# Kernel tuning notes

Measured on AMD Instinct MI355X. Metric: run time of the kernel, lower is better.

## Reference

```python
import jax, jax.numpy as jnp
import numpy as np

T, B, N, F = 128, 8, 32, 128
H = 256  # hidden channels
DEG = 8


def setup_inputs() -> dict:
    key = jax.random.key(0)
    ks = jax.random.split(key, 8)
    data = jax.random.normal(ks[0], (T, B, N, F), jnp.float32)
    all_ohs = jax.random.normal(ks[1], (T, B, N, 8), jnp.float32)
    n0 = B * N * T
    n1 = B * N * (T // 2)
    edge_index0 = jax.random.randint(ks[2], (2, n0 * DEG), 0, n0)
    edge_index1 = jax.random.randint(ks[3], (2, n1 * DEG), 0, n1)
    def init(k, shape, fan):
        return jax.random.normal(k, shape, jnp.float32) / np.float32(np.sqrt(fan))
    W0 = init(ks[4], (2 * F, H), 2 * F); b0 = jnp.zeros((H,), jnp.float32)
    Wc0 = init(ks[5], (H, H, 5), H * 5); bc0 = jnp.zeros((H,), jnp.float32)
    W1 = init(ks[6], (2 * H, H), 2 * H); b1 = jnp.zeros((H,), jnp.float32)
    Wc1 = init(ks[7], (H, H, 5), H * 5); bc1 = jnp.zeros((H,), jnp.float32)
    return dict(data=data, all_ohs=all_ohs,
                edge_index0=edge_index0, edge_index1=edge_index1,
                W0=W0, b0=b0, Wc0=Wc0, bc0=bc0,
                W1=W1, b1=b1, Wc1=Wc1, bc1=bc1)


def edge_conv(x, edge_index, W, b):
    # PyG EdgeConv: out_i = max_{(j->i)} relu(Linear(cat[x_i, x_j - x_i]))
    src, dst = edge_index[0], edge_index[1]
    x_i = x[dst]           # [E, C] target features
    x_j = x[src]           # [E, C] source features
    msg = jax.nn.relu(jnp.concatenate([x_i, x_j - x_i], axis=-1) @ W + b)
    out = jax.ops.segment_max(msg, dst, num_segments=x.shape[0])
    return jnp.where(jnp.isneginf(out), 0.0, out)  # empty segments -> 0 (PyG fill)


def temp_conv(x, Wc, bc):
    # x: [BN, C, L]; Conv1d(k=5, pad=2) + relu + MaxPool1d(2)
    y = jax.lax.conv_general_dilated(x, Wc, (1,), [(2, 2)],
                                     dimension_numbers=('NCH', 'OIH', 'NCH'))
    y = jax.nn.relu(y + bc[None, :, None])
    L2 = y.shape[-1] // 2
    y = y[..., : L2 * 2].reshape(y.shape[0], y.shape[1], L2, 2)
    return jnp.max(y, axis=-1)


def reference(data, all_ohs, edge_index0, edge_index1,
              W0, b0, Wc0, bc0, W1, b1, Wc1, bc1):
    # 'fast' path, context=False: all_ohs unused beyond reshape
    length = data.shape[0]
    x = data.reshape(T, B * N, F).transpose(1, 0, 2).reshape(-1, F)  # [BN*T, F]
    layers = ((edge_index0, W0, b0, Wc0, bc0),
              (edge_index1, W1, b1, Wc1, bc1))
    for ei, W, b, Wc, bc in layers:
        x = edge_conv(x, ei, W, b)                       # [BN*length, C]
        x = x.reshape(-1, length, x.shape[-1])           # [BN, length, C]
        x = x.transpose(0, 2, 1)                         # [BN, C, length]
        x = temp_conv(x, Wc, bc)                         # [BN, C, length//2]
        length = x.shape[2]
        C = x.shape[1]
        x = x.transpose(0, 2, 1).reshape(-1, C)          # [BN*length, C]
    return x
```

## Files before the change

kernel.cpp:

```cpp
#include <hip/hip_runtime.h>
#include <hip/hip_bf16.h>
#include <math.h>

#define T0 128
#define BN 256
#define Ff 128
#define Hh 256
#define NODE0 32768
#define E0 262144
#define T1 64
#define NODE1 16384
#define E1 131072
#define CAP 48

typedef __attribute__((ext_vector_type(8))) short bhalf8;
typedef __attribute__((ext_vector_type(4))) float floatx4;

__device__ __forceinline__ unsigned short f2bf(float x) {
  union { float f; unsigned u; } v; v.f = x;
  unsigned r = v.u + 0x7fff + ((v.u >> 16) & 1);
  return (unsigned short)(r >> 16);
}
__device__ __forceinline__ float bf2f(unsigned short b) {
  union { unsigned u; float f; } v; v.u = ((unsigned)b) << 16;
  return v.f;
}

__global__ void k_prep(const float* __restrict__ data, unsigned short* __restrict__ X0b,
                       const float* __restrict__ W0, unsigned short* __restrict__ Wbot0,
                       unsigned short* __restrict__ Wd0,
                       const float* __restrict__ W1, unsigned short* __restrict__ Wbot1,
                       unsigned short* __restrict__ Wd1,
                       const float* __restrict__ Wc0, unsigned short* __restrict__ Wtb0,
                       const float* __restrict__ Wc1, unsigned short* __restrict__ Wtb1) {
  int b = blockIdx.x;
  int tid = threadIdx.x;
  if (b < 2048) {
    int idx = b * 256 + tid;
    int c8 = idx & 15;
    int r  = idx >> 4;
    int t  = r & (T0 - 1);
    int bn = r >> 7;
    const float* s = data + ((size_t)t * BN + bn) * Ff + c8 * 8;
    float4 a = *(const float4*)s;
    float4 bb = *(const float4*)(s + 4);
    unsigned short o[8];
    o[0] = f2bf(a.x); o[1] = f2bf(a.y); o[2] = f2bf(a.z); o[3] = f2bf(a.w);
    o[4] = f2bf(bb.x); o[5] = f2bf(bb.y); o[6] = f2bf(bb.z); o[7] = f2bf(bb.w);
    *(int4*)(X0b + ((size_t)(bn * T0 + t) * Ff + c8 * 8)) = *(int4*)o;
  } else if (b < 2176) {
    int idx = (b - 2048) * 256 + tid;
    int n = idx >> 7, k = idx & 127;
    float top = W0[(size_t)k * 256 + n];
    float bot = W0[(size_t)(128 + k) * 256 + n];
    Wbot0[idx] = f2bf(bot);
    Wd0[idx]   = f2bf(top - bot);
  } else if (b < 2432) {
    int idx = (b - 2176) * 256 + tid;
    int n = idx >> 8, k = idx & 255;
    float top = W1[(size_t)k * 256 + n];
    float bot = W1[(size_t)(256 + k) * 256 + n];
    Wbot1[idx] = f2bf(bot);
    Wd1[idx]   = f2bf(top - bot);
  } else if (b < 3712) {
    int idx = (b - 2432) * 256 + tid;
    int tap = idx >> 16, o = (idx >> 8) & 255, i = idx & 255;
    Wtb0[idx] = f2bf(Wc0[((size_t)o * 256 + i) * 5 + tap]);
  } else {
    int idx = (b - 3712) * 256 + tid;
    int tap = idx >> 16, o = (idx >> 8) & 255, i = idx & 255;
    Wtb1[idx] = f2bf(Wc1[((size_t)o * 256 + i) * 5 + tap]);
  }
}


__global__ void k_fill(const int* __restrict__ srcIdx, const int* __restrict__ dstIdx,
                       int* __restrict__ cnt, int* __restrict__ slot, int E) {
  int e = blockIdx.x * 256 + threadIdx.x;
  if (e < E) {
    int d = dstIdx[e];
    int p = atomicAdd(&cnt[d], 1);
    if (p < CAP) slot[(size_t)d * CAP + p] = srcIdx[e];
  }
}

__global__ __launch_bounds__(256) void k_maxg(const unsigned short* __restrict__ Bm,
                                              const int* __restrict__ cnt,
                                              const int* __restrict__ slot,
                                              unsigned short* __restrict__ Mm) {
  int node = blockIdx.x * 4 + (threadIdx.x >> 6);
  int lane = threadIdx.x & 63;
  int n = cnt[node];
  if (n > CAP) n = CAP;
  const int* sl = slot + (size_t)node * CAP;
  float4 m = make_float4(-INFINITY, -INFINITY, -INFINITY, -INFINITY);
  int i = 0;
  for (; i + 4 <= n; i += 4) {
    int s0 = sl[i], s1 = sl[i + 1], s2 = sl[i + 2], s3 = sl[i + 3];
    ushort4 v0 = *(const ushort4*)(Bm + (size_t)s0 * 256 + lane * 4);
    ushort4 v1 = *(const ushort4*)(Bm + (size_t)s1 * 256 + lane * 4);
    ushort4 v2 = *(const ushort4*)(Bm + (size_t)s2 * 256 + lane * 4);
    ushort4 v3 = *(const ushort4*)(Bm + (size_t)s3 * 256 + lane * 4);
    m.x = fmaxf(fmaxf(fmaxf(m.x, bf2f(v0.x)), fmaxf(bf2f(v1.x), bf2f(v2.x))), bf2f(v3.x));
    m.y = fmaxf(fmaxf(fmaxf(m.y, bf2f(v0.y)), fmaxf(bf2f(v1.y), bf2f(v2.y))), bf2f(v3.y));
    m.z = fmaxf(fmaxf(fmaxf(m.z, bf2f(v0.z)), fmaxf(bf2f(v1.z), bf2f(v2.z))), bf2f(v3.z));
    m.w = fmaxf(fmaxf(fmaxf(m.w, bf2f(v0.w)), fmaxf(bf2f(v1.w), bf2f(v2.w))), bf2f(v3.w));
  }
  for (; i < n; ++i) {
    int s = sl[i];
    ushort4 v = *(const ushort4*)(Bm + (size_t)s * 256 + lane * 4);
    m.x = fmaxf(m.x, bf2f(v.x));
    m.y = fmaxf(m.y, bf2f(v.y));
    m.z = fmaxf(m.z, bf2f(v.z));
    m.w = fmaxf(m.w, bf2f(v.w));
  }
  ushort4 o;
  o.x = f2bf(m.x); o.y = f2bf(m.y); o.z = f2bf(m.z); o.w = f2bf(m.w);
  *(ushort4*)(Mm + (size_t)node * 256 + lane * 4) = o;
}

template <int MODE>
__global__ __launch_bounds__(256) void k_gemm(const unsigned short* __restrict__ A,
                                              const unsigned short* __restrict__ Wb,
                                              unsigned short* __restrict__ C, int K,
                                              const float* __restrict__ bias,
                                              const unsigned short* __restrict__ Mm) {
  __shared__ __align__(16) short A_lds[64 * 72];
  __shared__ __align__(16) short B_lds[128 * 72];
  int tid = threadIdx.x;
  int row0 = blockIdx.x * 64;
  int col0 = blockIdx.y * 128;
  int lane = tid & 63, wv = tid >> 6;
  int m16 = lane & 15, quad = lane >> 4;
  int sr = tid >> 3, sseg = tid & 7;

  floatx4 acc[8];
#pragma unroll
  for (int nt = 0; nt < 8; ++nt) acc[nt] = (floatx4){0.f, 0.f, 0.f, 0.f};

  for (int kb = 0; kb < K; kb += 64) {
    __syncthreads();
#pragma unroll
    for (int i = 0; i < 2; ++i) {
      int r = sr + i * 32;
      *(int4*)&A_lds[r * 72 + sseg * 8] =
          *(const int4*)(A + (size_t)(row0 + r) * K + kb + sseg * 8);
    }
#pragma unroll
    for (int i = 0; i < 4; ++i) {
      int r = sr + i * 32;
      *(int4*)&B_lds[r * 72 + sseg * 8] =
          *(const int4*)(Wb + (size_t)(col0 + r) * K + kb + sseg * 8);
    }
    __syncthreads();
#pragma unroll
    for (int ks = 0; ks < 2; ++ks) {
      bhalf8 a = *(const bhalf8*)&A_lds[(wv * 16 + m16) * 72 + ks * 32 + quad * 8];
#pragma unroll
      for (int nt = 0; nt < 8; ++nt) {
        bhalf8 b = *(const bhalf8*)&B_lds[(nt * 16 + m16) * 72 + ks * 32 + quad * 8];
        acc[nt] = __builtin_amdgcn_mfma_f32_16x16x32_bf16(a, b, acc[nt], 0, 0, 0);
      }
    }
  }

  int g0 = row0 + wv * 16 + quad * 4;
#pragma unroll
  for (int nt = 0; nt < 8; ++nt) {
    int c = col0 + nt * 16 + m16;
    float bv = (MODE == 1) ? bias[c] : 0.f;
#pragma unroll
    for (int r = 0; r < 4; ++r) {
      float v = acc[nt][r];
      if (MODE == 1) v = fmaxf(v + bv + bf2f(Mm[(size_t)(g0 + r) * 256 + c]), 0.f);
      C[(size_t)(g0 + r) * 256 + c] = f2bf(v);
    }
  }
}

template <int TRows, bool OUT_F32>
__global__ __launch_bounds__(256) void k_conv(const unsigned short* __restrict__ X,
                                              const unsigned short* __restrict__ Wtb,
                                              const float* __restrict__ bc,
                                              void* __restrict__ Yout) {
  const int rowTiles = TRows / 64;
  __shared__ __align__(16) short A_lds[68 * 72];
  __shared__ __align__(16) short B_lds[64 * 72];
  int tid = threadIdx.x;
  int bn = blockIdx.x / rowTiles;
  int t0 = (blockIdx.x % rowTiles) * 64;
  int col0 = blockIdx.y * 64;
  int lane = tid & 63, wv = tid >> 6;
  int m16 = lane & 15, quad = lane >> 4;
  int sr = tid >> 3, sseg = tid & 7;
  const unsigned short* Xbn = X + (size_t)bn * TRows * 256;

  floatx4 acc[4];
#pragma unroll
  for (int nt = 0; nt < 4; ++nt) acc[nt] = (floatx4){0.f, 0.f, 0.f, 0.f};

  for (int kb = 0; kb < 256; kb += 64) {
    __syncthreads();
    for (int u = tid; u < 68 * 8; u += 256) {
      int r = u >> 3, seg = u & 7;
      int t = t0 + r - 2;
      int4 v = {0, 0, 0, 0};
      if (t >= 0 && t < TRows)
        v = *(const int4*)(Xbn + (size_t)t * 256 + kb + seg * 8);
      *(int4*)&A_lds[r * 72 + seg * 8] = v;
    }
    for (int tap = 0; tap < 5; ++tap) {
      if (tap > 0) __syncthreads();
      const unsigned short* Wk = Wtb + (size_t)tap * 65536;
#pragma unroll
      for (int i = 0; i < 2; ++i) {
        int r = sr + i * 32;
        *(int4*)&B_lds[r * 72 + sseg * 8] =
            *(const int4*)(Wk + (size_t)(col0 + r) * 256 + kb + sseg * 8);
      }
      __syncthreads();
#pragma unroll
      for (int ks = 0; ks < 2; ++ks) {
        bhalf8 a = *(const bhalf8*)&A_lds[(wv * 16 + m16 + tap) * 72 + ks * 32 + quad * 8];
#pragma unroll
        for (int nt = 0; nt < 4; ++nt) {
          bhalf8 b = *(const bhalf8*)&B_lds[(nt * 16 + m16) * 72 + ks * 32 + quad * 8];
          acc[nt] = __builtin_amdgcn_mfma_f32_16x16x32_bf16(a, b, acc[nt], 0, 0, 0);
        }
      }
    }
  }

  int gbase = bn * TRows + t0 + wv * 16 + quad * 4;
#pragma unroll
  for (int nt = 0; nt < 4; ++nt) {
    int c = col0 + nt * 16 + m16;
    float bv = bc[c];
    float y0 = fmaxf(acc[nt][0] + bv, 0.f);
    float y1 = fmaxf(acc[nt][1] + bv, 0.f);
    float y2 = fmaxf(acc[nt][2] + bv, 0.f);
    float y3 = fmaxf(acc[nt][3] + bv, 0.f);
    float p0 = fmaxf(y0, y1);
    float p1 = fmaxf(y2, y3);
    int o0 = gbase >> 1;
    if (OUT_F32) {
      float* Y = (float*)Yout;
      Y[(size_t)o0 * 256 + c] = p0;
      Y[(size_t)(o0 + 1) * 256 + c] = p1;
    } else {
      unsigned short* Y = (unsigned short*)Yout;
      Y[(size_t)o0 * 256 + c] = f2bf(p0);
      Y[(size_t)(o0 + 1) * 256 + c] = f2bf(p1);
    }
  }
}

extern "C" void kernel_launch(void* const* d_in, const int* in_sizes, int n_in,
                              void* d_out, int out_size, void* d_ws, size_t ws_size,
                              hipStream_t stream) {
  const float* data = (const float*)d_in[0];
  const int* ei0 = (const int*)d_in[2];
  const int* ei1 = (const int*)d_in[3];
  const float* W0  = (const float*)d_in[4];
  const float* b0  = (const float*)d_in[5];
  const float* Wc0 = (const float*)d_in[6];
  const float* bc0 = (const float*)d_in[7];
  const float* W1  = (const float*)d_in[8];
  const float* b1  = (const float*)d_in[9];
  const float* Wc1 = (const float*)d_in[10];
  const float* bc1 = (const float*)d_in[11];
  float* out = (float*)d_out;

  char* base = (char*)d_ws;
  size_t off = 0;
  auto alloc = [&](size_t bytes) { void* p = base + off; off += (bytes + 255) & ~(size_t)255; return p; };
  unsigned short* X0b   = (unsigned short*)alloc((size_t)NODE0 * Ff * 2);
  unsigned short* Bm    = (unsigned short*)alloc((size_t)NODE0 * Hh * 2);
  unsigned short* Mm    = (unsigned short*)alloc((size_t)NODE0 * Hh * 2);
  unsigned short* X1b   = (unsigned short*)alloc((size_t)NODE0 * Hh * 2);
  unsigned short* Y0b   = (unsigned short*)alloc((size_t)NODE1 * Hh * 2);
  unsigned short* Wbot0 = (unsigned short*)alloc(256 * 128 * 2);
  unsigned short* Wd0   = (unsigned short*)alloc(256 * 128 * 2);
  unsigned short* Wbot1 = (unsigned short*)alloc(256 * 256 * 2);
  unsigned short* Wd1   = (unsigned short*)alloc(256 * 256 * 2);
  unsigned short* Wtb0  = (unsigned short*)alloc(5 * 65536 * 2);
  unsigned short* Wtb1  = (unsigned short*)alloc(5 * 65536 * 2);
  int* cnt0  = (int*)alloc(NODE0 * 4);
  int* cnt1  = (int*)alloc(NODE1 * 4);
  int* slot0 = (int*)alloc((size_t)NODE0 * CAP * 4);
  int* slot1 = (int*)alloc((size_t)NODE1 * CAP * 4);

  hipMemsetAsync(cnt0, 0, (NODE0 + NODE1) * sizeof(int), stream);

  k_prep<<<4992, 256, 0, stream>>>(data, X0b, W0, Wbot0, Wd0, W1, Wbot1, Wd1,
                                   Wc0, Wtb0, Wc1, Wtb1);

  k_fill<<<E0 / 256, 256, 0, stream>>>(ei0, ei0 + E0, cnt0, slot0, E0);
  k_gemm<0><<<dim3(NODE0 / 64, 2), 256, 0, stream>>>(X0b, Wbot0, Bm, 128, nullptr, nullptr);
  k_maxg<<<NODE0 / 4, 256, 0, stream>>>(Bm, cnt0, slot0, Mm);
  k_gemm<1><<<dim3(NODE0 / 64, 2), 256, 0, stream>>>(X0b, Wd0, X1b, 128, b0, Mm);
  k_conv<128, false><<<dim3(NODE0 / 64, 4), 256, 0, stream>>>(X1b, Wtb0, bc0, Y0b);

  k_fill<<<E1 / 256, 256, 0, stream>>>(ei1, ei1 + E1, cnt1, slot1, E1);
  k_gemm<0><<<dim3(NODE1 / 64, 2), 256, 0, stream>>>(Y0b, Wbot1, Bm, 256, nullptr, nullptr);
  k_maxg<<<NODE1 / 4, 256, 0, stream>>>(Bm, cnt1, slot1, Mm);
  k_gemm<1><<<dim3(NODE1 / 64, 2), 256, 0, stream>>>(Y0b, Wd1, X1b, 256, b1, Mm);
  k_conv<64, true><<<dim3(NODE1 / 64, 4), 256, 0, stream>>>(X1b, Wtb1, bc1, out);
}
```

Baseline: 258.5 us.

## Restructure temporal conv to load all five taps per K-slice and merge edge fills

The temporal conv kernel now processes 128 rows per block as two 64-row sub-tiles sharing each weight load. It stages all five tap weight slices for a 32-wide K chunk in LDS at once, which removes the per-tap barriers and doubles MFMA work per B fragment. The two edge-bucketing fill launches are merged into one kernel covering both graphs. The cost is more LDS per block and half as many conv blocks, which may reduce occupancy.

```diff
diff --git a/kernel.cpp b/kernel.cpp
--- a/kernel.cpp
+++ b/kernel.cpp
@@ -73,14 +73,19 @@
   }
 }
 
-
-__global__ void k_fill(const int* __restrict__ srcIdx, const int* __restrict__ dstIdx,
-                       int* __restrict__ cnt, int* __restrict__ slot, int E) {
+__global__ void k_fill(const int* __restrict__ ei0, const int* __restrict__ ei1,
+                       int* __restrict__ cnt0, int* __restrict__ cnt1,
+                       int* __restrict__ slot0, int* __restrict__ slot1) {
   int e = blockIdx.x * 256 + threadIdx.x;
-  if (e < E) {
-    int d = dstIdx[e];
-    int p = atomicAdd(&cnt[d], 1);
-    if (p < CAP) slot[(size_t)d * CAP + p] = srcIdx[e];
+  if (e < E0) {
+    int d = ei0[E0 + e];
+    int p = atomicAdd(&cnt0[d], 1);
+    if (p < CAP) slot0[(size_t)d * CAP + p] = ei0[e];
+  } else {
+    int e2 = e - E0;
+    int d = ei1[E1 + e2];
+    int p = atomicAdd(&cnt1[d], 1);
+    if (p < CAP) slot1[(size_t)d * CAP + p] = ei1[e2];
   }
 }
 
@@ -183,74 +188,79 @@
                                               const unsigned short* __restrict__ Wtb,
                                               const float* __restrict__ bc,
                                               void* __restrict__ Yout) {
-  const int rowTiles = TRows / 64;
-  __shared__ __align__(16) short A_lds[68 * 72];
-  __shared__ __align__(16) short B_lds[64 * 72];
+  __shared__ __align__(16) short A_lds[2 * 68 * 40];
+  __shared__ __align__(16) short B_lds[320 * 40];
   int tid = threadIdx.x;
-  int bn = blockIdx.x / rowTiles;
-  int t0 = (blockIdx.x % rowTiles) * 64;
+  int row0 = blockIdx.x * 128;
   int col0 = blockIdx.y * 64;
   int lane = tid & 63, wv = tid >> 6;
   int m16 = lane & 15, quad = lane >> 4;
-  int sr = tid >> 3, sseg = tid & 7;
-  const unsigned short* Xbn = X + (size_t)bn * TRows * 256;
-
-  floatx4 acc[4];
-#pragma unroll
-  for (int nt = 0; nt < 4; ++nt) acc[nt] = (floatx4){0.f, 0.f, 0.f, 0.f};
-
-  for (int kb = 0; kb < 256; kb += 64) {
+
+  floatx4 acc[2][4];
+#pragma unroll
+  for (int s = 0; s < 2; ++s)
+#pragma unroll
+    for (int nt = 0; nt < 4; ++nt) acc[s][nt] = (floatx4){0.f, 0.f, 0.f, 0.f};
+
+  for (int kb = 0; kb < 256; kb += 32) {
     __syncthreads();
-    for (int u = tid; u < 68 * 8; u += 256) {
-      int r = u >> 3, seg = u & 7;
-      int t = t0 + r - 2;
-      int4 v = {0, 0, 0, 0};
-      if (t >= 0 && t < TRows)
-        v = *(const int4*)(Xbn + (size_t)t * 256 + kb + seg * 8);
-      *(int4*)&A_lds[r * 72 + seg * 8] = v;
-    }
+    for (int u = tid; u < 544; u += 256) {
+      int s = (u >= 272) ? 1 : 0;
+      int v = u - s * 272;
+      int rr = v >> 2, seg = v & 3;
+      int base = row0 + s * 64;
+      int lo = base & ~(TRows - 1);
+      int g = base + rr - 2;
+      int4 val = {0, 0, 0, 0};
+      if (g >= lo && g < lo + TRows)
+        val = *(const int4*)(X + (size_t)g * 256 + kb + seg * 8);
+      *(int4*)&A_lds[(s * 68 + rr) * 40 + seg * 8] = val;
+    }
+#pragma unroll
+    for (int i = 0; i < 5; ++i) {
+      int u = tid + i * 256;
+      int r = u >> 2, seg = u & 3;
+      int tap = r >> 6, col = r & 63;
+      *(int4*)&B_lds[r * 40 + seg * 8] =
+          *(const int4*)(Wtb + (size_t)tap * 65536 + (size_t)(col0 + col) * 256 + kb + seg * 8);
+    }
+    __syncthreads();
+#pragma unroll
     for (int tap = 0; tap < 5; ++tap) {
-      if (tap > 0) __syncthreads();
-      const unsigned short* Wk = Wtb + (size_t)tap * 65536;
-#pragma unroll
-      for (int i = 0; i < 2; ++i) {
-        int r = sr + i * 32;
-        *(int4*)&B_lds[r * 72 + sseg * 8] =
-            *(const int4*)(Wk + (size_t)(col0 + r) * 256 + kb + sseg * 8);
+      bhalf8 a0 = *(const bhalf8*)&A_lds[(wv * 16 + m16 + tap) * 40 + quad * 8];
+      bhalf8 a1 = *(const bhalf8*)&A_lds[(68 + wv * 16 + m16 + tap) * 40 + quad * 8];
+#pragma unroll
+      for (int nt = 0; nt < 4; ++nt) {
+        bhalf8 b = *(const bhalf8*)&B_lds[((tap << 6) + nt * 16 + m16) * 40 + quad * 8];
+        acc[0][nt] = __builtin_amdgcn_mfma_f32_16x16x32_bf16(a0, b, acc[0][nt], 0, 0, 0);
+        acc[1][nt] = __builtin_amdgcn_mfma_f32_16x16x32_bf16(a1, b, acc[1][nt], 0, 0, 0);
       }
-      __syncthreads();
-#pragma unroll
-      for (int ks = 0; ks < 2; ++ks) {
-        bhalf8 a = *(const bhalf8*)&A_lds[(wv * 16 + m16 + tap) * 72 + ks * 32 + quad * 8];
-#pragma unroll
-        for (int nt = 0; nt < 4; ++nt) {
-          bhalf8 b = *(const bhalf8*)&B_lds[(nt * 16 + m16) * 72 + ks * 32 + quad * 8];
-          acc[nt] = __builtin_amdgcn_mfma_f32_16x16x32_bf16(a, b, acc[nt], 0, 0, 0);
-        }
+    }
+  }
+
+#pragma unroll
+  for (int s = 0; s < 2; ++s) {
+    int gbase = row0 + s * 64 + wv * 16 + quad * 4;
+#pragma unroll
+    for (int nt = 0; nt < 4; ++nt) {
+      int c = col0 + nt * 16 + m16;
+      float bv = bc[c];
+      float y0 = fmaxf(acc[s][nt][0] + bv, 0.f);
+      float y1 = fmaxf(acc[s][nt][1] + bv, 0.f);
+      float y2 = fmaxf(acc[s][nt][2] + bv, 0.f);
+      float y3 = fmaxf(acc[s][nt][3] + bv, 0.f);
+      float p0 = fmaxf(y0, y1);
+      float p1 = fmaxf(y2, y3);
+      int o0 = gbase >> 1;
+      if (OUT_F32) {
+        float* Y = (float*)Yout;
+        Y[(size_t)o0 * 256 + c] = p0;
+        Y[(size_t)(o0 + 1) * 256 + c] = p1;
+      } else {
+        unsigned short* Y = (unsigned short*)Yout;
+        Y[(size_t)o0 * 256 + c] = f2bf(p0);
+        Y[(size_t)(o0 + 1) * 256 + c] = f2bf(p1);
       }
-    }
-  }
-
-  int gbase = bn * TRows + t0 + wv * 16 + quad * 4;
-#pragma unroll
-  for (int nt = 0; nt < 4; ++nt) {
-    int c = col0 + nt * 16 + m16;
-    float bv = bc[c];
-    float y0 = fmaxf(acc[nt][0] + bv, 0.f);
-    float y1 = fmaxf(acc[nt][1] + bv, 0.f);
-    float y2 = fmaxf(acc[nt][2] + bv, 0.f);
-    float y3 = fmaxf(acc[nt][3] + bv, 0.f);
-    float p0 = fmaxf(y0, y1);
-    float p1 = fmaxf(y2, y3);
-    int o0 = gbase >> 1;
-    if (OUT_F32) {
-      float* Y = (float*)Yout;
-      Y[(size_t)o0 * 256 + c] = p0;
-      Y[(size_t)(o0 + 1) * 256 + c] = p1;
-    } else {
-      unsigned short* Y = (unsigned short*)Yout;
-      Y[(size_t)o0 * 256 + c] = f2bf(p0);
-      Y[(size_t)(o0 + 1) * 256 + c] = f2bf(p1);
     }
   }
 }
@@ -294,16 +304,15 @@
 
   k_prep<<<4992, 256, 0, stream>>>(data, X0b, W0, Wbot0, Wd0, W1, Wbot1, Wd1,
                                    Wc0, Wtb0, Wc1, Wtb1);
-
-  k_fill<<<E0 / 256, 256, 0, stream>>>(ei0, ei0 + E0, cnt0, slot0, E0);
+  k_fill<<<(E0 + E1) / 256, 256, 0, stream>>>(ei0, ei1, cnt0, cnt1, slot0, slot1);
+
   k_gemm<0><<<dim3(NODE0 / 64, 2), 256, 0, stream>>>(X0b, Wbot0, Bm, 128, nullptr, nullptr);
   k_maxg<<<NODE0 / 4, 256, 0, stream>>>(Bm, cnt0, slot0, Mm);
   k_gemm<1><<<dim3(NODE0 / 64, 2), 256, 0, stream>>>(X0b, Wd0, X1b, 128, b0, Mm);
-  k_conv<128, false><<<dim3(NODE0 / 64, 4), 256, 0, stream>>>(X1b, Wtb0, bc0, Y0b);
-
-  k_fill<<<E1 / 256, 256, 0, stream>>>(ei1, ei1 + E1, cnt1, slot1, E1);
+  k_conv<128, false><<<dim3(NODE0 / 128, 4), 256, 0, stream>>>(X1b, Wtb0, bc0, Y0b);
+
   k_gemm<0><<<dim3(NODE1 / 64, 2), 256, 0, stream>>>(Y0b, Wbot1, Bm, 256, nullptr, nullptr);
   k_maxg<<<NODE1 / 4, 256, 0, stream>>>(Bm, cnt1, slot1, Mm);
   k_gemm<1><<<dim3(NODE1 / 64, 2), 256, 0, stream>>>(Y0b, Wd1, X1b, 256, b1, Mm);
-  k_conv<64, true><<<dim3(NODE1 / 64, 4), 256, 0, stream>>>(X1b, Wtb1, bc1, out);
-}
+  k_conv<64, true><<<dim3(NODE1 / 128, 4), 256, 0, stream>>>(X1b, Wtb1, bc1, out);
+}
```

Measured after the change: 249.0 us. -3.7%, faster.
